# Performance work log

Hardware: AMD Instinct MI355X
Metric: run time of the kernel (lower is better)

## Reference

```python
import jax, jax.numpy as jnp
import numpy as np

B_SZ, LAT, ADIM, MAXA, DM, DI, NST, NB = 8192, 64, 16, 9, 128, 256, 16, 2


def _layernorm(x, g, b, eps=1e-5):
    mu = x.mean(-1, keepdims=True)
    var = ((x - mu) ** 2).mean(-1, keepdims=True)
    return (x - mu) / jnp.sqrt(var + eps) * g + b


def _ssm_block(x, h, ng, nb, in_w, xp_w, logA, dt_bias, Dv, out_w):
    # x: (B, DM), h: (B, DI, NST)
    residual = x
    xn = _layernorm(x, ng, nb)
    xz = xn @ in_w.T                      # (B, 2*DI)
    x_main, z = jnp.split(xz, 2, axis=-1)  # (B, DI) each
    xp = x_main @ xp_w.T                  # (B, 2*NST+1)
    B_t = xp[:, :NST]                     # (B, NST)
    C_t = xp[:, NST:2 * NST]              # (B, NST)
    delta = jax.nn.softplus(xp[:, -1:] + dt_bias)      # (B, DI)
    A = jnp.exp(logA)                                  # (DI, NST)
    A_bar = jnp.exp(-delta[..., None] * A)             # (B, DI, NST)
    B_bar = delta[..., None] * B_t[:, None, :]         # (B, DI, NST)
    h_new = A_bar * h + B_bar * x_main[..., None]      # (B, DI, NST)
    y = jnp.einsum('bdn,bn->bd', h_new, C_t) + Dv * x_main
    y = y * jax.nn.silu(z)
    y = y @ out_w.T + residual
    return y, h_new


def setup_inputs() -> dict:
    key = jax.random.key(0)
    ks = jax.random.split(key, 24)
    rn = lambda k, s, sc=0.05: jax.random.normal(k, s, jnp.float32) * sc
    log_A = -jnp.log(jnp.arange(1, NST + 1, dtype=jnp.float32))  # (NST,)
    return {
        'z_t': jax.random.normal(ks[0], (B_SZ, LAT), jnp.float32),
        'action': jax.random.randint(ks[1], (B_SZ,), 0, MAXA),
        'h': jax.random.normal(ks[2], (NB, B_SZ, DI, NST), jnp.float32),
        'action_embed': rn(ks[3], (MAXA, ADIM), 1.0),
        'fusion_w': rn(ks[4], (DM, LAT + ADIM)),
        'fusion_b': jnp.zeros((DM,), jnp.float32),
        'norm_g': jnp.ones((NB, DM), jnp.float32),
        'norm_b': jnp.zeros((NB, DM), jnp.float32),
        'in_proj_w': rn(ks[5], (NB, 2 * DI, DM)),
        'x_proj_w': rn(ks[6], (NB, 2 * NST + 1, DI)),
        'log_A': jnp.broadcast_to(log_A, (NB, DI, NST)) + jnp.zeros((NB, DI, NST), jnp.float32),
        'dt_bias': rn(ks[7], (NB, DI), 0.01) - 2.0,
        'Dp': jnp.ones((NB, DI), jnp.float32),
        'out_proj_w': rn(ks[8], (NB, DM, DI)),
        'ns_w1': rn(ks[9], (DM, DM)), 'ns_b1': jnp.zeros((DM,), jnp.float32),
        'ns_w2': rn(ks[10], (LAT, DM)), 'ns_b2': jnp.zeros((LAT,), jnp.float32),
        'rw_w1': rn(ks[11], (DM // 2, DM)), 'rw_b1': jnp.zeros((DM // 2,), jnp.float32),
        'rw_w2': rn(ks[12], (1, DM // 2)), 'rw_b2': jnp.zeros((1,), jnp.float32),
        'dn_w1': rn(ks[13], (DM // 2, DM)), 'dn_b1': jnp.zeros((DM // 2,), jnp.float32),
        'dn_w2': rn(ks[14], (1, DM // 2)), 'dn_b2': jnp.zeros((1,), jnp.float32),
    }


def reference(z_t, action, h, action_embed, fusion_w, fusion_b, norm_g, norm_b,
              in_proj_w, x_proj_w, log_A, dt_bias, Dp, out_proj_w,
              ns_w1, ns_b1, ns_w2, ns_b2, rw_w1, rw_b1, rw_w2, rw_b2,
              dn_w1, dn_b1, dn_w2, dn_b2):
    a_emb = action_embed[action]                               # (B, ADIM)
    x = jax.nn.relu(jnp.concatenate([z_t, a_emb], -1) @ fusion_w.T + fusion_b)
    new_h = []
    for i in range(NB):  # fixed small number of structurally-distinct blocks
        x, h_i = _ssm_block(x, h[i], norm_g[i], norm_b[i], in_proj_w[i],
                            x_proj_w[i], log_A[i], dt_bias[i], Dp[i], out_proj_w[i])
        new_h.append(h_i)
    h_new = jnp.stack(new_h)                                   # (NB, B, DI, NST)
    z_next = jax.nn.relu(x @ ns_w1.T + ns_b1) @ ns_w2.T + ns_b2
    reward = jax.nn.relu(x @ rw_w1.T + rw_b1) @ rw_w2.T + rw_b2
    done_logit = jax.nn.relu(x @ dn_w1.T + dn_b1) @ dn_w2.T + dn_b2
    return (z_next, reward, done_logit, h_new)
```

## Files before the change

kernel.cpp:

```cpp
#include <hip/hip_runtime.h>

#define B_SZ 8192
#define LAT  64
#define ADIM 16
#define DM   128
#define DI   256
#define NST  16
#define NB   2
#define ROWS 8
#define NT   256

#define Z_OFF  0
#define RW_OFF (B_SZ * LAT)
#define DN_OFF (RW_OFF + B_SZ)
#define H_OFF  (DN_OFF + B_SZ)

__device__ __forceinline__ float softplus_f(float v) {
    return fmaxf(v, 0.f) + log1pf(__expf(-fabsf(v)));
}
__device__ __forceinline__ float silu_f(float z) {
    return z / (1.f + __expf(-z));
}
__device__ __forceinline__ float dot4(float4 a, float4 b, float acc) {
    acc = fmaf(a.x, b.x, acc);
    acc = fmaf(a.y, b.y, acc);
    acc = fmaf(a.z, b.z, acc);
    acc = fmaf(a.w, b.w, acc);
    return acc;
}

__global__ __launch_bounds__(NT) void mamba_wm_kernel(
    const float* __restrict__ z_t,
    const int*   __restrict__ action,
    const float* __restrict__ h_in,
    const float* __restrict__ a_embed,
    const float* __restrict__ fusion_w,
    const float* __restrict__ fusion_b,
    const float* __restrict__ norm_g,
    const float* __restrict__ norm_b,
    const float* __restrict__ in_proj_w,
    const float* __restrict__ x_proj_w,
    const float* __restrict__ log_A,
    const float* __restrict__ dt_bias,
    const float* __restrict__ Dp,
    const float* __restrict__ out_proj_w,
    const float* __restrict__ ns_w1, const float* __restrict__ ns_b1,
    const float* __restrict__ ns_w2, const float* __restrict__ ns_b2,
    const float* __restrict__ rw_w1, const float* __restrict__ rw_b1,
    const float* __restrict__ rw_w2, const float* __restrict__ rw_b2,
    const float* __restrict__ dn_w1, const float* __restrict__ dn_b1,
    const float* __restrict__ dn_w2, const float* __restrict__ dn_b2,
    float* __restrict__ out)
{
    __shared__ __align__(16) float s_x [ROWS][132];
    __shared__ __align__(16) float s_xn[ROWS][132];
    __shared__ __align__(16) float s_xm[ROWS][260];
    __shared__ __align__(16) float s_z [ROWS][260];
    __shared__ __align__(16) float s_xp[ROWS][36];

    const int t    = threadIdx.x;
    const int row0 = blockIdx.x * ROWS;

    for (int idx = t; idx < ROWS * 80; idx += NT) {
        int r = idx / 80;
        int k = idx - r * 80;
        int row = row0 + r;
        float v;
        if (k < LAT) v = z_t[(size_t)row * LAT + k];
        else         v = a_embed[action[row] * ADIM + (k - LAT)];
        s_xn[r][k] = v;
    }
    __syncthreads();

    {
        const int j  = t & 127;
        const int rb = t >> 7;
        const float* wrow = fusion_w + j * 80;
        float acc[4];
        #pragma unroll
        for (int rr = 0; rr < 4; ++rr) acc[rr] = fusion_b[j];
        for (int k = 0; k < 80; k += 4) {
            float4 w4 = *reinterpret_cast<const float4*>(wrow + k);
            #pragma unroll
            for (int rr = 0; rr < 4; ++rr) {
                int r = rb + 2 * rr;
                float4 x4 = *reinterpret_cast<const float4*>(&s_xn[r][k]);
                acc[rr] = dot4(w4, x4, acc[rr]);
            }
        }
        #pragma unroll
        for (int rr = 0; rr < 4; ++rr)
            s_x[rb + 2 * rr][j] = fmaxf(acc[rr], 0.f);
    }
    __syncthreads();

    for (int blk = 0; blk < NB; ++blk) {
        const float* ng  = norm_g     + blk * DM;
        const float* nbv = norm_b     + blk * DM;
        const float* inw = in_proj_w  + (size_t)blk * 2 * DI * DM;
        const float* xpw = x_proj_w   + (size_t)blk * 33 * DI;
        const float* lA  = log_A      + (size_t)blk * DI * NST;
        const float* dtb = dt_bias    + blk * DI;
        const float* dpv = Dp         + blk * DI;
        const float* ow  = out_proj_w + (size_t)blk * DM * DI;

        {
            const int r = t >> 5;
            const int l = t & 31;
            float s = 0.f;
            #pragma unroll
            for (int m = 0; m < 4; ++m) s += s_x[r][l + 32 * m];
            #pragma unroll
            for (int m = 1; m < 32; m <<= 1) s += __shfl_xor(s, m, 32);
            float mu = s * (1.f / 128.f);
            float v = 0.f;
            #pragma unroll
            for (int m = 0; m < 4; ++m) {
                float d = s_x[r][l + 32 * m] - mu;
                v = fmaf(d, d, v);
            }
            #pragma unroll
            for (int m = 1; m < 32; m <<= 1) v += __shfl_xor(v, m, 32);
            float rstd = 1.f / sqrtf(v * (1.f / 128.f) + 1e-5f);
            #pragma unroll
            for (int m = 0; m < 4; ++m) {
                int k = l + 32 * m;
                s_xn[r][k] = (s_x[r][k] - mu) * rstd * ng[k] + nbv[k];
            }
        }
        __syncthreads();

        {
            const float* wa = inw + (size_t)t * DM;
            const float* wb = inw + (size_t)(t + DI) * DM;
            float aa[ROWS], ab[ROWS];
            #pragma unroll
            for (int r = 0; r < ROWS; ++r) { aa[r] = 0.f; ab[r] = 0.f; }
            for (int k = 0; k < DM; k += 4) {
                float4 w4a = *reinterpret_cast<const float4*>(wa + k);
                float4 w4b = *reinterpret_cast<const float4*>(wb + k);
                #pragma unroll
                for (int r = 0; r < ROWS; ++r) {
                    float4 x4 = *reinterpret_cast<const float4*>(&s_xn[r][k]);
                    aa[r] = dot4(w4a, x4, aa[r]);
                    ab[r] = dot4(w4b, x4, ab[r]);
                }
            }
            #pragma unroll
            for (int r = 0; r < ROWS; ++r) {
                s_xm[r][t] = aa[r];
                s_z [r][t] = ab[r];
            }
        }
        __syncthreads();

        for (int it = t; it < ROWS * 33; it += NT) {
            int r = it / 33;
            int j = it - r * 33;
            const float* w = xpw + (size_t)j * DI;
            float acc = 0.f;
            for (int k = 0; k < DI; k += 4) {
                float4 w4 = *reinterpret_cast<const float4*>(w + k);
                float4 x4 = *reinterpret_cast<const float4*>(&s_xm[r][k]);
                acc = dot4(w4, x4, acc);
            }
            s_xp[r][j] = acc;
        }
        __syncthreads();

        {
            const int d = t;
            float Av[NST];
            #pragma unroll
            for (int n = 0; n < NST; ++n) Av[n] = __expf(lA[d * NST + n]);
            const float dtbd = dtb[d];
            const float Dvd  = dpv[d];
            const float* hbase = h_in + (((size_t)blk * B_SZ + row0) * DI + d) * NST;
            float*       obase = out + H_OFF + (((size_t)blk * B_SZ + row0) * DI + d) * NST;

            float4 p0 = *reinterpret_cast<const float4*>(hbase + 0);
            float4 p1 = *reinterpret_cast<const float4*>(hbase + 4);
            float4 p2 = *reinterpret_cast<const float4*>(hbase + 8);
            float4 p3 = *reinterpret_cast<const float4*>(hbase + 12);

            for (int r = 0; r < ROWS; ++r) {
                float4 q0 = p0, q1 = p1, q2 = p2, q3 = p3;
                if (r + 1 < ROWS) {
                    const float* hn = hbase + (size_t)(r + 1) * DI * NST;
                    p0 = *reinterpret_cast<const float4*>(hn + 0);
                    p1 = *reinterpret_cast<const float4*>(hn + 4);
                    p2 = *reinterpret_cast<const float4*>(hn + 8);
                    p3 = *reinterpret_cast<const float4*>(hn + 12);
                }
                float xm    = s_xm[r][d];
                float zz    = s_z [r][d];
                float delta = softplus_f(s_xp[r][32] + dtbd);
                float dxm   = delta * xm;

                float hv[16], Bv[16], Cv[16];
                *reinterpret_cast<float4*>(hv + 0)  = q0;
                *reinterpret_cast<float4*>(hv + 4)  = q1;
                *reinterpret_cast<float4*>(hv + 8)  = q2;
                *reinterpret_cast<float4*>(hv + 12) = q3;
                *reinterpret_cast<float4*>(Bv + 0)  = *reinterpret_cast<const float4*>(&s_xp[r][0]);
                *reinterpret_cast<float4*>(Bv + 4)  = *reinterpret_cast<const float4*>(&s_xp[r][4]);
                *reinterpret_cast<float4*>(Bv + 8)  = *reinterpret_cast<const float4*>(&s_xp[r][8]);
                *reinterpret_cast<float4*>(Bv + 12) = *reinterpret_cast<const float4*>(&s_xp[r][12]);
                *reinterpret_cast<float4*>(Cv + 0)  = *reinterpret_cast<const float4*>(&s_xp[r][16]);
                *reinterpret_cast<float4*>(Cv + 4)  = *reinterpret_cast<const float4*>(&s_xp[r][20]);
                *reinterpret_cast<float4*>(Cv + 8)  = *reinterpret_cast<const float4*>(&s_xp[r][24]);
                *reinterpret_cast<float4*>(Cv + 12) = *reinterpret_cast<const float4*>(&s_xp[r][28]);

                float y = 0.f;
                #pragma unroll
                for (int n = 0; n < 16; ++n) {
                    float ab = __expf(-delta * Av[n]);
                    float hn = fmaf(ab, hv[n], dxm * Bv[n]);
                    y = fmaf(hn, Cv[n], y);
                    hv[n] = hn;
                }
                float* ho = obase + (size_t)r * DI * NST;
                *reinterpret_cast<float4*>(ho + 0)  = *reinterpret_cast<float4*>(hv + 0);
                *reinterpret_cast<float4*>(ho + 4)  = *reinterpret_cast<float4*>(hv + 4);
                *reinterpret_cast<float4*>(ho + 8)  = *reinterpret_cast<float4*>(hv + 8);
                *reinterpret_cast<float4*>(ho + 12) = *reinterpret_cast<float4*>(hv + 12);

                y = fmaf(Dvd, xm, y);
                s_xm[r][d] = y * silu_f(zz);
            }
        }
        __syncthreads();

        {
            const int j  = t & 127;
            const int rb = t >> 7;
            const float* w = ow + (size_t)j * DI;
            float acc[4];
            #pragma unroll
            for (int rr = 0; rr < 4; ++rr) acc[rr] = 0.f;
            for (int k = 0; k < DI; k += 4) {
                float4 w4 = *reinterpret_cast<const float4*>(w + k);
                #pragma unroll
                for (int rr = 0; rr < 4; ++rr) {
                    int r = rb + 2 * rr;
                    float4 x4 = *reinterpret_cast<const float4*>(&s_xm[r][k]);
                    acc[rr] = dot4(w4, x4, acc[rr]);
                }
            }
            #pragma unroll
            for (int rr = 0; rr < 4; ++rr) {
                int r = rb + 2 * rr;
                s_x[r][j] += acc[rr];
            }
        }
        __syncthreads();
    }

    {
        const int j  = t & 127;
        const int rb = t >> 7;
        const float* w = ns_w1 + (size_t)j * DM;
        float acc[4];
        #pragma unroll
        for (int rr = 0; rr < 4; ++rr) acc[rr] = ns_b1[j];
        for (int k = 0; k < DM; k += 4) {
            float4 w4 = *reinterpret_cast<const float4*>(w + k);
            #pragma unroll
            for (int rr = 0; rr < 4; ++rr) {
                int r = rb + 2 * rr;
                float4 x4 = *reinterpret_cast<const float4*>(&s_x[r][k]);
                acc[rr] = dot4(w4, x4, acc[rr]);
            }
        }
        #pragma unroll
        for (int rr = 0; rr < 4; ++rr)
            s_xn[rb + 2 * rr][j] = fmaxf(acc[rr], 0.f);
    }
    {
        const int o   = t & 63;
        const int rb4 = t >> 6;
        const float* wr = rw_w1 + (size_t)o * DM;
        const float* wd = dn_w1 + (size_t)o * DM;
        float accR[2], accD[2];
        #pragma unroll
        for (int m = 0; m < 2; ++m) { accR[m] = rw_b1[o]; accD[m] = dn_b1[o]; }
        for (int k = 0; k < DM; k += 4) {
            float4 w4r = *reinterpret_cast<const float4*>(wr + k);
            float4 w4d = *reinterpret_cast<const float4*>(wd + k);
            #pragma unroll
            for (int m = 0; m < 2; ++m) {
                int r = rb4 + 4 * m;
                float4 x4 = *reinterpret_cast<const float4*>(&s_x[r][k]);
                accR[m] = dot4(w4r, x4, accR[m]);
                accD[m] = dot4(w4d, x4, accD[m]);
            }
        }
        #pragma unroll
        for (int m = 0; m < 2; ++m) {
            int r = rb4 + 4 * m;
            s_z [r][o] = fmaxf(accR[m], 0.f);
            s_xm[r][o] = fmaxf(accD[m], 0.f);
        }
    }
    __syncthreads();

    {
        const int o   = t & 63;
        const int rb4 = t >> 6;
        const float* w = ns_w2 + (size_t)o * DM;
        float acc[2];
        #pragma unroll
        for (int m = 0; m < 2; ++m) acc[m] = ns_b2[o];
        for (int k = 0; k < DM; k += 4) {
            float4 w4 = *reinterpret_cast<const float4*>(w + k);
            #pragma unroll
            for (int m = 0; m < 2; ++m) {
                int r = rb4 + 4 * m;
                float4 x4 = *reinterpret_cast<const float4*>(&s_xn[r][k]);
                acc[m] = dot4(w4, x4, acc[m]);
            }
        }
        #pragma unroll
        for (int m = 0; m < 2; ++m) {
            int r = rb4 + 4 * m;
            out[Z_OFF + (size_t)(row0 + r) * LAT + o] = acc[m];
        }
    }
    if (t < 16) {
        const int r    = t & 7;
        const bool isR = (t < 8);
        const float* w2 = isR ? rw_w2 : dn_w2;
        const float  b2 = isR ? rw_b2[0] : dn_b2[0];
        float acc = b2;
        if (isR) {
            for (int k = 0; k < 64; ++k) acc = fmaf(s_z[r][k], w2[k], acc);
            out[RW_OFF + row0 + r] = acc;
        } else {
            for (int k = 0; k < 64; ++k) acc = fmaf(s_xm[r][k], w2[k], acc);
            out[DN_OFF + row0 + r] = acc;
        }
    }
}

extern "C" void kernel_launch(void* const* d_in, const int* in_sizes, int n_in,
                              void* d_out, int out_size, void* d_ws, size_t ws_size,
                              hipStream_t stream) {
    (void)in_sizes; (void)n_in; (void)out_size; (void)d_ws; (void)ws_size;
    mamba_wm_kernel<<<B_SZ / ROWS, NT, 0, stream>>>(
        (const float*)d_in[0],  (const int*)d_in[1],   (const float*)d_in[2],
        (const float*)d_in[3],  (const float*)d_in[4], (const float*)d_in[5],
        (const float*)d_in[6],  (const float*)d_in[7], (const float*)d_in[8],
        (const float*)d_in[9],  (const float*)d_in[10],(const float*)d_in[11],
        (const float*)d_in[12], (const float*)d_in[13],(const float*)d_in[14],
        (const float*)d_in[15], (const float*)d_in[16],(const float*)d_in[17],
        (const float*)d_in[18], (const float*)d_in[19],(const float*)d_in[20],
        (const float*)d_in[21], (const float*)d_in[22],(const float*)d_in[23],
        (const float*)d_in[24], (const float*)d_in[25],
        (float*)d_out);
}
```

Baseline: 731.6 us.

## Split fused kernel into staged kernels with a per-row SSM scan kernel

The single fused per-8-row kernel is split into five launches: a projection kernel, a one-block-per-row SSM state update, a middle kernel that does out_proj plus the next block's projections, a second SSM pass, and a post kernel for the heads. Intermediates (x, x_main, z, xp) are staged through the global workspace. Dense stages now use 16 rows and 512 threads, and the bandwidth-heavy h update gets 8192 blocks, which aims to raise occupancy and memory parallelism on the h stream. In exchange it adds workspace round-trips, extra launch overhead and per-row reloads of log_A.

Measured after the change: 753.6 us. 3.0% more time.

```diff
diff --git a/kernel.cpp b/kernel.cpp
--- a/kernel.cpp
+++ b/kernel.cpp
@@ -7,13 +7,17 @@
 #define DI   256
 #define NST  16
 #define NB   2
-#define ROWS 8
-#define NT   256
+#define ROWS 16
 
 #define Z_OFF  0
 #define RW_OFF (B_SZ * LAT)
 #define DN_OFF (RW_OFF + B_SZ)
 #define H_OFF  (DN_OFF + B_SZ)
+
+#define WS_X0 0
+#define WS_XM (B_SZ * DM)
+#define WS_Z  (WS_XM + B_SZ * DI)
+#define WS_XP (WS_Z + B_SZ * DI)
 
 __device__ __forceinline__ float softplus_f(float v) {
     return fmaxf(v, 0.f) + log1pf(__expf(-fabsf(v)));
@@ -29,20 +33,276 @@
     return acc;
 }
 
-__global__ __launch_bounds__(NT) void mamba_wm_kernel(
-    const float* __restrict__ z_t,
-    const int*   __restrict__ action,
-    const float* __restrict__ h_in,
+__global__ __launch_bounds__(512) void k_pre(
+    const float* __restrict__ z_t, const int* __restrict__ action,
     const float* __restrict__ a_embed,
-    const float* __restrict__ fusion_w,
-    const float* __restrict__ fusion_b,
-    const float* __restrict__ norm_g,
-    const float* __restrict__ norm_b,
-    const float* __restrict__ in_proj_w,
-    const float* __restrict__ x_proj_w,
-    const float* __restrict__ log_A,
-    const float* __restrict__ dt_bias,
-    const float* __restrict__ Dp,
+    const float* __restrict__ fusion_w, const float* __restrict__ fusion_b,
+    const float* __restrict__ norm_g, const float* __restrict__ norm_b,
+    const float* __restrict__ in_proj_w, const float* __restrict__ x_proj_w,
+    float* __restrict__ ws)
+{
+    __shared__ __align__(16) float s_in[ROWS][84];
+    __shared__ __align__(16) float s_x [ROWS][132];
+    __shared__ __align__(16) float s_xn[ROWS][132];
+    __shared__ __align__(16) float s_xm[ROWS][260];
+    const int t    = threadIdx.x;
+    const int row0 = blockIdx.x * ROWS;
+
+    for (int idx = t; idx < ROWS * 80; idx += 512) {
+        int r = idx / 80, k = idx - r * 80;
+        int row = row0 + r;
+        s_in[r][k] = (k < LAT) ? z_t[(size_t)row * LAT + k]
+                               : a_embed[action[row] * ADIM + (k - LAT)];
+    }
+    __syncthreads();
+
+    {
+        const int j  = t & 127;
+        const int rb = t >> 7;
+        const float* wrow = fusion_w + j * 80;
+        float acc[4];
+        #pragma unroll
+        for (int rr = 0; rr < 4; ++rr) acc[rr] = fusion_b[j];
+        for (int k = 0; k < 80; k += 4) {
+            float4 w4 = *reinterpret_cast<const float4*>(wrow + k);
+            #pragma unroll
+            for (int rr = 0; rr < 4; ++rr) {
+                float4 x4 = *reinterpret_cast<const float4*>(&s_in[rb + 4 * rr][k]);
+                acc[rr] = dot4(w4, x4, acc[rr]);
+            }
+        }
+        #pragma unroll
+        for (int rr = 0; rr < 4; ++rr) {
+            int r = rb + 4 * rr;
+            float v = fmaxf(acc[rr], 0.f);
+            s_x[r][j] = v;
+            ws[WS_X0 + (size_t)(row0 + r) * DM + j] = v;
+        }
+    }
+    __syncthreads();
+
+    {
+        const int r = t >> 5, l = t & 31;
+        float s = 0.f;
+        #pragma unroll
+        for (int m = 0; m < 4; ++m) s += s_x[r][l + 32 * m];
+        #pragma unroll
+        for (int m = 1; m < 32; m <<= 1) s += __shfl_xor(s, m, 32);
+        float mu = s * (1.f / 128.f);
+        float v = 0.f;
+        #pragma unroll
+        for (int m = 0; m < 4; ++m) { float d = s_x[r][l + 32 * m] - mu; v = fmaf(d, d, v); }
+        #pragma unroll
+        for (int m = 1; m < 32; m <<= 1) v += __shfl_xor(v, m, 32);
+        float rstd = 1.f / sqrtf(v * (1.f / 128.f) + 1e-5f);
+        #pragma unroll
+        for (int m = 0; m < 4; ++m) {
+            int k = l + 32 * m;
+            s_xn[r][k] = (s_x[r][k] - mu) * rstd * norm_g[k] + norm_b[k];
+        }
+    }
+    __syncthreads();
+
+    {
+        const float* w = in_proj_w + (size_t)t * DM;
+        float acc[ROWS];
+        #pragma unroll
+        for (int r = 0; r < ROWS; ++r) acc[r] = 0.f;
+        for (int k = 0; k < DM; k += 4) {
+            float4 w4 = *reinterpret_cast<const float4*>(w + k);
+            #pragma unroll
+            for (int r = 0; r < ROWS; ++r) {
+                float4 x4 = *reinterpret_cast<const float4*>(&s_xn[r][k]);
+                acc[r] = dot4(w4, x4, acc[r]);
+            }
+        }
+        if (t < DI) {
+            #pragma unroll
+            for (int r = 0; r < ROWS; ++r) {
+                s_xm[r][t] = acc[r];
+                ws[WS_XM + (size_t)(row0 + r) * DI + t] = acc[r];
+            }
+        } else {
+            #pragma unroll
+            for (int r = 0; r < ROWS; ++r)
+                ws[WS_Z + (size_t)(row0 + r) * DI + (t - DI)] = acc[r];
+        }
+    }
+    __syncthreads();
+
+    for (int it = t; it < ROWS * 33; it += 512) {
+        int r = it / 33, j = it - r * 33;
+        const float* w = x_proj_w + (size_t)j * DI;
+        float acc = 0.f;
+        for (int k = 0; k < DI; k += 4) {
+            float4 w4 = *reinterpret_cast<const float4*>(w + k);
+            float4 x4 = *reinterpret_cast<const float4*>(&s_xm[r][k]);
+            acc = dot4(w4, x4, acc);
+        }
+        ws[WS_XP + (size_t)(row0 + r) * 36 + j] = acc;
+    }
+}
+
+__global__ __launch_bounds__(256) void k_ssm(
+    const float* __restrict__ h_in, const float* __restrict__ log_A,
+    const float* __restrict__ dt_bias, const float* __restrict__ Dp,
+    float* __restrict__ ws, float* __restrict__ out, int blk)
+{
+    __shared__ float s_xp[36];
+    const int t   = threadIdx.x;
+    const int row = blockIdx.x;
+    if (t < 36) s_xp[t] = ws[WS_XP + (size_t)row * 36 + t];
+    __syncthreads();
+
+    const int d = t;
+    const float* lA = log_A + ((size_t)blk * DI + d) * NST;
+    float Av[NST];
+    #pragma unroll
+    for (int n = 0; n < NST; ++n) Av[n] = __expf(lA[n]);
+
+    const float xm    = ws[WS_XM + (size_t)row * DI + d];
+    const float zz    = ws[WS_Z  + (size_t)row * DI + d];
+    const float delta = softplus_f(s_xp[32] + dt_bias[blk * DI + d]);
+    const float dxm   = delta * xm;
+
+    const size_t hoff = ((size_t)(blk * B_SZ + row) * DI + d) * NST;
+    const float* hb = h_in + hoff;
+    float hv[NST];
+    *reinterpret_cast<float4*>(hv + 0)  = *reinterpret_cast<const float4*>(hb + 0);
+    *reinterpret_cast<float4*>(hv + 4)  = *reinterpret_cast<const float4*>(hb + 4);
+    *reinterpret_cast<float4*>(hv + 8)  = *reinterpret_cast<const float4*>(hb + 8);
+    *reinterpret_cast<float4*>(hv + 12) = *reinterpret_cast<const float4*>(hb + 12);
+
+    float y = 0.f;
+    #pragma unroll
+    for (int n = 0; n < NST; ++n) {
+        float ab = __expf(-delta * Av[n]);
+        float hn = fmaf(ab, hv[n], dxm * s_xp[n]);
+        y = fmaf(hn, s_xp[16 + n], y);
+        hv[n] = hn;
+    }
+    float* ho = out + H_OFF + hoff;
+    *reinterpret_cast<float4*>(ho + 0)  = *reinterpret_cast<float4*>(hv + 0);
+    *reinterpret_cast<float4*>(ho + 4)  = *reinterpret_cast<float4*>(hv + 4);
+    *reinterpret_cast<float4*>(ho + 8)  = *reinterpret_cast<float4*>(hv + 8);
+    *reinterpret_cast<float4*>(ho + 12) = *reinterpret_cast<float4*>(hv + 12);
+
+    y = fmaf(Dp[blk * DI + d], xm, y);
+    ws[WS_XM + (size_t)row * DI + d] = y * silu_f(zz);
+}
+
+__global__ __launch_bounds__(512) void k_mid(
+    const float* __restrict__ norm_g, const float* __restrict__ norm_b,
+    const float* __restrict__ in_proj_w, const float* __restrict__ x_proj_w,
+    const float* __restrict__ out_proj_w, float* __restrict__ ws)
+{
+    __shared__ __align__(16) float s_y [ROWS][260];
+    __shared__ __align__(16) float s_x [ROWS][132];
+    __shared__ __align__(16) float s_xn[ROWS][132];
+    __shared__ __align__(16) float s_xm[ROWS][260];
+    const int t    = threadIdx.x;
+    const int row0 = blockIdx.x * ROWS;
+
+    for (int idx = t; idx < ROWS * 64; idx += 512) {
+        int r = idx >> 6, c = (idx & 63) * 4;
+        *reinterpret_cast<float4*>(&s_y[r][c]) =
+            *reinterpret_cast<const float4*>(&ws[WS_XM + (size_t)(row0 + r) * DI + c]);
+    }
+    for (int idx = t; idx < ROWS * 32; idx += 512) {
+        int r = idx >> 5, c = (idx & 31) * 4;
+        *reinterpret_cast<float4*>(&s_x[r][c]) =
+            *reinterpret_cast<const float4*>(&ws[WS_X0 + (size_t)(row0 + r) * DM + c]);
+    }
+    __syncthreads();
+
+    {
+        const int j  = t & 127;
+        const int rb = t >> 7;
+        const float* w = out_proj_w + (size_t)j * DI;
+        float acc[4] = {0.f, 0.f, 0.f, 0.f};
+        for (int k = 0; k < DI; k += 4) {
+            float4 w4 = *reinterpret_cast<const float4*>(w + k);
+            #pragma unroll
+            for (int rr = 0; rr < 4; ++rr) {
+                float4 x4 = *reinterpret_cast<const float4*>(&s_y[rb + 4 * rr][k]);
+                acc[rr] = dot4(w4, x4, acc[rr]);
+            }
+        }
+        #pragma unroll
+        for (int rr = 0; rr < 4; ++rr) {
+            int r = rb + 4 * rr;
+            float v = s_x[r][j] + acc[rr];
+            s_x[r][j] = v;
+            ws[WS_X0 + (size_t)(row0 + r) * DM + j] = v;
+        }
+    }
+    __syncthreads();
+
+    {
+        const int r = t >> 5, l = t & 31;
+        const float* ng  = norm_g + DM;
+        const float* nbv = norm_b + DM;
+        float s = 0.f;
+        #pragma unroll
+        for (int m = 0; m < 4; ++m) s += s_x[r][l + 32 * m];
+        #pragma unroll
+        for (int m = 1; m < 32; m <<= 1) s += __shfl_xor(s, m, 32);
+        float mu = s * (1.f / 128.f);
+        float v = 0.f;
+        #pragma unroll
+        for (int m = 0; m < 4; ++m) { float d = s_x[r][l + 32 * m] - mu; v = fmaf(d, d, v); }
+        #pragma unroll
+        for (int m = 1; m < 32; m <<= 1) v += __shfl_xor(v, m, 32);
+        float rstd = 1.f / sqrtf(v * (1.f / 128.f) + 1e-5f);
+        #pragma unroll
+        for (int m = 0; m < 4; ++m) {
+            int k = l + 32 * m;
+            s_xn[r][k] = (s_x[r][k] - mu) * rstd * ng[k] + nbv[k];
+        }
+    }
+    __syncthreads();
+
+    {
+        const float* w = in_proj_w + (size_t)(2 * DI * DM) + (size_t)t * DM;
+        float acc[ROWS];
+        #pragma unroll
+        for (int r = 0; r < ROWS; ++r) acc[r] = 0.f;
+        for (int k = 0; k < DM; k += 4) {
+            float4 w4 = *reinterpret_cast<const float4*>(w + k);
+            #pragma unroll
+            for (int r = 0; r < ROWS; ++r) {
+                float4 x4 = *reinterpret_cast<const float4*>(&s_xn[r][k]);
+                acc[r] = dot4(w4, x4, acc[r]);
+            }
+        }
+        if (t < DI) {
+            #pragma unroll
+            for (int r = 0; r < ROWS; ++r) {
+                s_xm[r][t] = acc[r];
+                ws[WS_XM + (size_t)(row0 + r) * DI + t] = acc[r];
+            }
+        } else {
+            #pragma unroll
+            for (int r = 0; r < ROWS; ++r)
+                ws[WS_Z + (size_t)(row0 + r) * DI + (t - DI)] = acc[r];
+        }
+    }
+    __syncthreads();
+
+    for (int it = t; it < ROWS * 33; it += 512) {
+        int r = it / 33, j = it - r * 33;
+        const float* w = x_proj_w + (size_t)(33 * DI) + (size_t)j * DI;
+        float acc = 0.f;
+        for (int k = 0; k < DI; k += 4) {
+            float4 w4 = *reinterpret_cast<const float4*>(w + k);
+            float4 x4 = *reinterpret_cast<const float4*>(&s_xm[r][k]);
+            acc = dot4(w4, x4, acc);
+        }
+        ws[WS_XP + (size_t)(row0 + r) * 36 + j] = acc;
+    }
+}
+
+__global__ __launch_bounds__(512) void k_post(
     const float* __restrict__ out_proj_w,
     const float* __restrict__ ns_w1, const float* __restrict__ ns_b1,
     const float* __restrict__ ns_w2, const float* __restrict__ ns_b2,
@@ -50,211 +310,46 @@
     const float* __restrict__ rw_w2, const float* __restrict__ rw_b2,
     const float* __restrict__ dn_w1, const float* __restrict__ dn_b1,
     const float* __restrict__ dn_w2, const float* __restrict__ dn_b2,
-    float* __restrict__ out)
+    float* __restrict__ ws, float* __restrict__ out)
 {
+    __shared__ __align__(16) float s_y [ROWS][260];
     __shared__ __align__(16) float s_x [ROWS][132];
     __shared__ __align__(16) float s_xn[ROWS][132];
-    __shared__ __align__(16) float s_xm[ROWS][260];
-    __shared__ __align__(16) float s_z [ROWS][260];
-    __shared__ __align__(16) float s_xp[ROWS][36];
-
     const int t    = threadIdx.x;
     const int row0 = blockIdx.x * ROWS;
 
-    for (int idx = t; idx < ROWS * 80; idx += NT) {
-        int r = idx / 80;
-        int k = idx - r * 80;
-        int row = row0 + r;
-        float v;
-        if (k < LAT) v = z_t[(size_t)row * LAT + k];
-        else         v = a_embed[action[row] * ADIM + (k - LAT)];
-        s_xn[r][k] = v;
+    for (int idx = t; idx < ROWS * 64; idx += 512) {
+        int r = idx >> 6, c = (idx & 63) * 4;
+        *reinterpret_cast<float4*>(&s_y[r][c]) =
+            *reinterpret_cast<const float4*>(&ws[WS_XM + (size_t)(row0 + r) * DI + c]);
+    }
+    for (int idx = t; idx < ROWS * 32; idx += 512) {
+        int r = idx >> 5, c = (idx & 31) * 4;
+        *reinterpret_cast<float4*>(&s_x[r][c]) =
+            *reinterpret_cast<const float4*>(&ws[WS_X0 + (size_t)(row0 + r) * DM + c]);
     }
     __syncthreads();
 
     {
         const int j  = t & 127;
         const int rb = t >> 7;
-        const float* wrow = fusion_w + j * 80;
-        float acc[4];
-        #pragma unroll
-        for (int rr = 0; rr < 4; ++rr) acc[rr] = fusion_b[j];
-        for (int k = 0; k < 80; k += 4) {
-            float4 w4 = *reinterpret_cast<const float4*>(wrow + k);
+        const float* w = out_proj_w + (size_t)(DM * DI) + (size_t)j * DI;
+        float acc[4] = {0.f, 0.f, 0.f, 0.f};
+        for (int k = 0; k < DI; k += 4) {
+            float4 w4 = *reinterpret_cast<const float4*>(w + k);
             #pragma unroll
             for (int rr = 0; rr < 4; ++rr) {
-                int r = rb + 2 * rr;
-                float4 x4 = *reinterpret_cast<const float4*>(&s_xn[r][k]);
+                float4 x4 = *reinterpret_cast<const float4*>(&s_y[rb + 4 * rr][k]);
                 acc[rr] = dot4(w4, x4, acc[rr]);
             }
         }
         #pragma unroll
-        for (int rr = 0; rr < 4; ++rr)
-            s_x[rb + 2 * rr][j] = fmaxf(acc[rr], 0.f);
-    }
-    __syncthreads();
-
-    for (int blk = 0; blk < NB; ++blk) {
-        const float* ng  = norm_g     + blk * DM;
-        const float* nbv = norm_b     + blk * DM;
-        const float* inw = in_proj_w  + (size_t)blk * 2 * DI * DM;
-        const float* xpw = x_proj_w   + (size_t)blk * 33 * DI;
-        const float* lA  = log_A      + (size_t)blk * DI * NST;
-        const float* dtb = dt_bias    + blk * DI;
-        const float* dpv = Dp         + blk * DI;
-        const float* ow  = out_proj_w + (size_t)blk * DM * DI;
-
-        {
-            const int r = t >> 5;
-            const int l = t & 31;
-            float s = 0.f;
-            #pragma unroll
-            for (int m = 0; m < 4; ++m) s += s_x[r][l + 32 * m];
-            #pragma unroll
-            for (int m = 1; m < 32; m <<= 1) s += __shfl_xor(s, m, 32);
-            float mu = s * (1.f / 128.f);
-            float v = 0.f;
-            #pragma unroll
-            for (int m = 0; m < 4; ++m) {
-                float d = s_x[r][l + 32 * m] - mu;
-                v = fmaf(d, d, v);
-            }
-            #pragma unroll
-            for (int m = 1; m < 32; m <<= 1) v += __shfl_xor(v, m, 32);
-            float rstd = 1.f / sqrtf(v * (1.f / 128.f) + 1e-5f);
-            #pragma unroll
-            for (int m = 0; m < 4; ++m) {
-                int k = l + 32 * m;
-                s_xn[r][k] = (s_x[r][k] - mu) * rstd * ng[k] + nbv[k];
-            }
-        }
-        __syncthreads();
-
-        {
-            const float* wa = inw + (size_t)t * DM;
-            const float* wb = inw + (size_t)(t + DI) * DM;
-            float aa[ROWS], ab[ROWS];
-            #pragma unroll
-            for (int r = 0; r < ROWS; ++r) { aa[r] = 0.f; ab[r] = 0.f; }
-            for (int k = 0; k < DM; k += 4) {
-                float4 w4a = *reinterpret_cast<const float4*>(wa + k);
-                float4 w4b = *reinterpret_cast<const float4*>(wb + k);
-                #pragma unroll
-                for (int r = 0; r < ROWS; ++r) {
-                    float4 x4 = *reinterpret_cast<const float4*>(&s_xn[r][k]);
-                    aa[r] = dot4(w4a, x4, aa[r]);
-                    ab[r] = dot4(w4b, x4, ab[r]);
-                }
-            }
-            #pragma unroll
-            for (int r = 0; r < ROWS; ++r) {
-                s_xm[r][t] = aa[r];
-                s_z [r][t] = ab[r];
-            }
-        }
-        __syncthreads();
-
-        for (int it = t; it < ROWS * 33; it += NT) {
-            int r = it / 33;
-            int j = it - r * 33;
-            const float* w = xpw + (size_t)j * DI;
-            float acc = 0.f;
-            for (int k = 0; k < DI; k += 4) {
-                float4 w4 = *reinterpret_cast<const float4*>(w + k);
-                float4 x4 = *reinterpret_cast<const float4*>(&s_xm[r][k]);
-                acc = dot4(w4, x4, acc);
-            }
-            s_xp[r][j] = acc;
-        }
-        __syncthreads();
-
-        {
-            const int d = t;
-            float Av[NST];
-            #pragma unroll
-            for (int n = 0; n < NST; ++n) Av[n] = __expf(lA[d * NST + n]);
-            const float dtbd = dtb[d];
-            const float Dvd  = dpv[d];
-            const float* hbase = h_in + (((size_t)blk * B_SZ + row0) * DI + d) * NST;
-            float*       obase = out + H_OFF + (((size_t)blk * B_SZ + row0) * DI + d) * NST;
-
-            float4 p0 = *reinterpret_cast<const float4*>(hbase + 0);
-            float4 p1 = *reinterpret_cast<const float4*>(hbase + 4);
-            float4 p2 = *reinterpret_cast<const float4*>(hbase + 8);
-            float4 p3 = *reinterpret_cast<const float4*>(hbase + 12);
-
-            for (int r = 0; r < ROWS; ++r) {
-                float4 q0 = p0, q1 = p1, q2 = p2, q3 = p3;
-                if (r + 1 < ROWS) {
-                    const float* hn = hbase + (size_t)(r + 1) * DI * NST;
-                    p0 = *reinterpret_cast<const float4*>(hn + 0);
-                    p1 = *reinterpret_cast<const float4*>(hn + 4);
-                    p2 = *reinterpret_cast<const float4*>(hn + 8);
-                    p3 = *reinterpret_cast<const float4*>(hn + 12);
-                }
-                float xm    = s_xm[r][d];
-                float zz    = s_z [r][d];
-                float delta = softplus_f(s_xp[r][32] + dtbd);
-                float dxm   = delta * xm;
-
-                float hv[16], Bv[16], Cv[16];
-                *reinterpret_cast<float4*>(hv + 0)  = q0;
-                *reinterpret_cast<float4*>(hv + 4)  = q1;
-                *reinterpret_cast<float4*>(hv + 8)  = q2;
-                *reinterpret_cast<float4*>(hv + 12) = q3;
-                *reinterpret_cast<float4*>(Bv + 0)  = *reinterpret_cast<const float4*>(&s_xp[r][0]);
-                *reinterpret_cast<float4*>(Bv + 4)  = *reinterpret_cast<const float4*>(&s_xp[r][4]);
-                *reinterpret_cast<float4*>(Bv + 8)  = *reinterpret_cast<const float4*>(&s_xp[r][8]);
-                *reinterpret_cast<float4*>(Bv + 12) = *reinterpret_cast<const float4*>(&s_xp[r][12]);
-                *reinterpret_cast<float4*>(Cv + 0)  = *reinterpret_cast<const float4*>(&s_xp[r][16]);
-                *reinterpret_cast<float4*>(Cv + 4)  = *reinterpret_cast<const float4*>(&s_xp[r][20]);
-                *reinterpret_cast<float4*>(Cv + 8)  = *reinterpret_cast<const float4*>(&s_xp[r][24]);
-                *reinterpret_cast<float4*>(Cv + 12) = *reinterpret_cast<const float4*>(&s_xp[r][28]);
-
-                float y = 0.f;
-                #pragma unroll
-                for (int n = 0; n < 16; ++n) {
-                    float ab = __expf(-delta * Av[n]);
-                    float hn = fmaf(ab, hv[n], dxm * Bv[n]);
-                    y = fmaf(hn, Cv[n], y);
-                    hv[n] = hn;
-                }
-                float* ho = obase + (size_t)r * DI * NST;
-                *reinterpret_cast<float4*>(ho + 0)  = *reinterpret_cast<float4*>(hv + 0);
-                *reinterpret_cast<float4*>(ho + 4)  = *reinterpret_cast<float4*>(hv + 4);
-                *reinterpret_cast<float4*>(ho + 8)  = *reinterpret_cast<float4*>(hv + 8);
-                *reinterpret_cast<float4*>(ho + 12) = *reinterpret_cast<float4*>(hv + 12);
-
-                y = fmaf(Dvd, xm, y);
-                s_xm[r][d] = y * silu_f(zz);
-            }
-        }
-        __syncthreads();
-
-        {
-            const int j  = t & 127;
-            const int rb = t >> 7;
-            const float* w = ow + (size_t)j * DI;
-            float acc[4];
-            #pragma unroll
-            for (int rr = 0; rr < 4; ++rr) acc[rr] = 0.f;
-            for (int k = 0; k < DI; k += 4) {
-                float4 w4 = *reinterpret_cast<const float4*>(w + k);
-                #pragma unroll
-                for (int rr = 0; rr < 4; ++rr) {
-                    int r = rb + 2 * rr;
-                    float4 x4 = *reinterpret_cast<const float4*>(&s_xm[r][k]);
-                    acc[rr] = dot4(w4, x4, acc[rr]);
-                }
-            }
-            #pragma unroll
-            for (int rr = 0; rr < 4; ++rr) {
-                int r = rb + 2 * rr;
-                s_x[r][j] += acc[rr];
-            }
-        }
-        __syncthreads();
-    }
+        for (int rr = 0; rr < 4; ++rr) {
+            int r = rb + 4 * rr;
+            s_x[r][j] += acc[rr];
+        }
+    }
+    __syncthreads();
 
     {
         const int j  = t & 127;
@@ -267,18 +362,17 @@
             float4 w4 = *reinterpret_cast<const float4*>(w + k);
             #pragma unroll
             for (int rr = 0; rr < 4; ++rr) {
-                int r = rb + 2 * rr;
-                float4 x4 = *reinterpret_cast<const float4*>(&s_x[r][k]);
+                float4 x4 = *reinterpret_cast<const float4*>(&s_x[rb + 4 * rr][k]);
                 acc[rr] = dot4(w4, x4, acc[rr]);
             }
         }
         #pragma unroll
         for (int rr = 0; rr < 4; ++rr)
-            s_xn[rb + 2 * rr][j] = fmaxf(acc[rr], 0.f);
+            s_xn[rb + 4 * rr][j] = fmaxf(acc[rr], 0.f);
     }
     {
         const int o   = t & 63;
-        const int rb4 = t >> 6;
+        const int rb8 = t >> 6;
         const float* wr = rw_w1 + (size_t)o * DM;
         const float* wd = dn_w1 + (size_t)o * DM;
         float accR[2], accD[2];
@@ -289,24 +383,23 @@
             float4 w4d = *reinterpret_cast<const float4*>(wd + k);
             #pragma unroll
             for (int m = 0; m < 2; ++m) {
-                int r = rb4 + 4 * m;
-                float4 x4 = *reinterpret_cast<const float4*>(&s_x[r][k]);
+                float4 x4 = *reinterpret_cast<const float4*>(&s_x[rb8 + 8 * m][k]);
                 accR[m] = dot4(w4r, x4, accR[m]);
                 accD[m] = dot4(w4d, x4, accD[m]);
             }
         }
         #pragma unroll
         for (int m = 0; m < 2; ++m) {
-            int r = rb4 + 4 * m;
-            s_z [r][o] = fmaxf(accR[m], 0.f);
-            s_xm[r][o] = fmaxf(accD[m], 0.f);
+            int r = rb8 + 8 * m;
+            s_y[r][o]       = fmaxf(accR[m], 0.f);
+            s_y[r][128 + o] = fmaxf(accD[m], 0.f);
         }
     }
     __syncthreads();
 
     {
         const int o   = t & 63;
-        const int rb4 = t >> 6;
+        const int rb8 = t >> 6;
         const float* w = ns_w2 + (size_t)o * DM;
         float acc[2];
         #pragma unroll
@@ -315,46 +408,55 @@
             float4 w4 = *reinterpret_cast<const float4*>(w + k);
             #pragma unroll
             for (int m = 0; m < 2; ++m) {
-                int r = rb4 + 4 * m;
-                float4 x4 = *reinterpret_cast<const float4*>(&s_xn[r][k]);
+                float4 x4 = *reinterpret_cast<const float4*>(&s_xn[rb8 + 8 * m][k]);
                 acc[m] = dot4(w4, x4, acc[m]);
             }
         }
         #pragma unroll
         for (int m = 0; m < 2; ++m) {
-            int r = rb4 + 4 * m;
+            int r = rb8 + 8 * m;
             out[Z_OFF + (size_t)(row0 + r) * LAT + o] = acc[m];
         }
     }
-    if (t < 16) {
-        const int r    = t & 7;
-        const bool isR = (t < 8);
+    if (t < 32) {
+        const int r    = t & 15;
+        const bool isR = (t < 16);
         const float* w2 = isR ? rw_w2 : dn_w2;
         const float  b2 = isR ? rw_b2[0] : dn_b2[0];
+        const int    co = isR ? 0 : 128;
         float acc = b2;
-        if (isR) {
-            for (int k = 0; k < 64; ++k) acc = fmaf(s_z[r][k], w2[k], acc);
-            out[RW_OFF + row0 + r] = acc;
-        } else {
-            for (int k = 0; k < 64; ++k) acc = fmaf(s_xm[r][k], w2[k], acc);
-            out[DN_OFF + row0 + r] = acc;
-        }
+        for (int k = 0; k < 64; ++k) acc = fmaf(s_y[r][co + k], w2[k], acc);
+        out[(isR ? RW_OFF : DN_OFF) + row0 + r] = acc;
     }
 }
 
 extern "C" void kernel_launch(void* const* d_in, const int* in_sizes, int n_in,
                               void* d_out, int out_size, void* d_ws, size_t ws_size,
                               hipStream_t stream) {
-    (void)in_sizes; (void)n_in; (void)out_size; (void)d_ws; (void)ws_size;
-    mamba_wm_kernel<<<B_SZ / ROWS, NT, 0, stream>>>(
-        (const float*)d_in[0],  (const int*)d_in[1],   (const float*)d_in[2],
-        (const float*)d_in[3],  (const float*)d_in[4], (const float*)d_in[5],
-        (const float*)d_in[6],  (const float*)d_in[7], (const float*)d_in[8],
-        (const float*)d_in[9],  (const float*)d_in[10],(const float*)d_in[11],
-        (const float*)d_in[12], (const float*)d_in[13],(const float*)d_in[14],
-        (const float*)d_in[15], (const float*)d_in[16],(const float*)d_in[17],
-        (const float*)d_in[18], (const float*)d_in[19],(const float*)d_in[20],
-        (const float*)d_in[21], (const float*)d_in[22],(const float*)d_in[23],
-        (const float*)d_in[24], (const float*)d_in[25],
-        (float*)d_out);
-}
+    (void)in_sizes; (void)n_in; (void)out_size; (void)ws_size;
+    const float* z_t      = (const float*)d_in[0];
+    const int*   action   = (const int*)  d_in[1];
+    const float* h_in     = (const float*)d_in[2];
+    const float* a_embed  = (const float*)d_in[3];
+    const float* norm_g   = (const float*)d_in[6];
+    const float* norm_b   = (const float*)d_in[7];
+    const float* in_w     = (const float*)d_in[8];
+    const float* xp_w     = (const float*)d_in[9];
+    const float* log_A    = (const float*)d_in[10];
+    const float* dt_bias  = (const float*)d_in[11];
+    const float* Dp       = (const float*)d_in[12];
+    const float* out_w    = (const float*)d_in[13];
+    float* ws  = (float*)d_ws;
+    float* out = (float*)d_out;
+
+    k_pre<<<B_SZ / ROWS, 512, 0, stream>>>(z_t, action, a_embed,
+        (const float*)d_in[4], (const float*)d_in[5], norm_g, norm_b, in_w, xp_w, ws);
+    k_ssm<<<B_SZ, 256, 0, stream>>>(h_in, log_A, dt_bias, Dp, ws, out, 0);
+    k_mid<<<B_SZ / ROWS, 512, 0, stream>>>(norm_g, norm_b, in_w, xp_w, out_w, ws);
+    k_ssm<<<B_SZ, 256, 0, stream>>>(h_in, log_A, dt_bias, Dp, ws, out, 1);
+    k_post<<<B_SZ / ROWS, 512, 0, stream>>>(out_w,
+        (const float*)d_in[14], (const float*)d_in[15], (const float*)d_in[16], (const float*)d_in[17],
+        (const float*)d_in[18], (const float*)d_in[19], (const float*)d_in[20], (const float*)d_in[21],
+        (const float*)d_in[22], (const float*)d_in[23], (const float*)d_in[24], (const float*)d_in[25],
+        ws, out);
+}
```
